# Performance work log

Measured on AMD Instinct MI355X. Metric: run time of the kernel, lower is better.

## Reference

```python
import jax, jax.numpy as jnp
import numpy as np

N_FINE = 1_000_000
N_COARSE = 250_000
K = 9            # filter extent for pos_dim=3 lattice coarsening: 2*(pos_dim+1)+1
C_IN = 64
C_OUT = 64       # nr_filters


def setup_inputs() -> dict:
    key = jax.random.key(0)
    k1, k2, k3, k4 = jax.random.split(key, 4)
    lv = jax.random.normal(k1, (N_FINE, C_IN), dtype=jnp.float32)
    # neighbor indices of each coarse vertex into the fine vertex array;
    # real lattice uses -1 for missing neighbors, emulated by masking in reference
    neighbor_idx = jax.random.randint(k2, (N_COARSE, K), 0, N_FINE, dtype=jnp.int64)
    W = jax.random.normal(k3, (K * C_IN, C_OUT), dtype=jnp.float32) * (1.0 / np.sqrt(K * C_IN))
    b = jax.random.normal(k4, (C_OUT,), dtype=jnp.float32) * 0.01
    return {"lv": lv, "neighbor_idx": neighbor_idx, "W": W, "b": b}


def reference(lv, neighbor_idx, W, b):
    # ReluCoarsen.forward: relu on lattice values, then lattice coarsening conv.
    x = jax.nn.relu(lv)                                   # [N_fine, C_in]
    valid = neighbor_idx >= 0                             # missing-neighbor mask
    idx = jnp.maximum(neighbor_idx, 0)
    gathered = x[idx]                                     # [N_coarse, K, C_in] (irregular gather)
    gathered = jnp.where(valid[:, :, None], gathered, 0.0)
    rows = gathered.reshape(gathered.shape[0], K * C_IN)  # im2row
    lv_1 = rows @ W + b                                   # [N_coarse, C_out]
    return lv_1
```

## Files before the change

### kernel.cpp

```cpp
#include <hip/hip_runtime.h>

#define N_COARSE_C 250000
#define KNB 9
#define CIN 64
#define COUT 64
#define NKK 18

typedef __attribute__((ext_vector_type(8))) short short8;
typedef __attribute__((ext_vector_type(4))) float f32x4;

__device__ __forceinline__ unsigned short f2bf(float x) {
    __bf16 h = (__bf16)x;
    return __builtin_bit_cast(unsigned short, h);
}

__global__ __launch_bounds__(512, 4) void relu_coarsen_mfma(
    const float* __restrict__ lv,
    const int*   __restrict__ nbr,
    const float* __restrict__ W,
    const float* __restrict__ bias,
    float*       __restrict__ out)
{
    __shared__ short wf[NKK * 4 * 64 * 8];

    const int tid = threadIdx.x;

    for (int p = tid; p < (576 * 64) / 2; p += 512) {
        const int n  = p & 63;
        const int k  = (p >> 6) * 2;
        const float a0 = W[k * 64 + n];
        const float a1 = W[(k + 1) * 64 + n];
        const unsigned pk = (unsigned)f2bf(a0) | ((unsigned)f2bf(a1) << 16);
        const int kk = k >> 5;
        const int gq = (k >> 3) & 3;
        const int e  = k & 7;
        const int sidx = ((kk * 4 + (n >> 4)) * 64 + gq * 16 + (n & 15)) * 8 + e;
        *reinterpret_cast<unsigned*>(&wf[sidx]) = pk;
    }
    __syncthreads();

    const int lane = tid & 63;
    const int wave = tid >> 6;
    const int m    = lane & 15;
    const int g    = lane >> 4;

    const int c0 = blockIdx.x * 128 + wave * 16;
    int c = c0 + m;
    if (c >= N_COARSE_C) c = N_COARSE_C - 1;

    int nb[KNB];
    #pragma unroll
    for (int j = 0; j < KNB; ++j) nb[j] = nbr[c * KNB + j];

    f32x4 acc[4];
    #pragma unroll
    for (int nt = 0; nt < 4; ++nt) acc[nt] = (f32x4){0.f, 0.f, 0.f, 0.f};

    #pragma unroll
    for (int kk = 0; kk < NKK; ++kk) {
        const int j  = kk >> 1;
        const int cb = ((kk & 1) << 5) + g * 8;
        const int row = nb[j];
        short8 a;
        if (row >= 0) {
            const f32x4* src = reinterpret_cast<const f32x4*>(
                lv + (size_t)row * CIN + cb);
            f32x4 v0 = src[0];
            f32x4 v1 = src[1];
            #pragma unroll
            for (int e = 0; e < 4; ++e) {
                a[e]     = (short)f2bf(fmaxf(v0[e], 0.f));
                a[e + 4] = (short)f2bf(fmaxf(v1[e], 0.f));
            }
        } else {
            #pragma unroll
            for (int e = 0; e < 8; ++e) a[e] = (short)0;
        }
        #pragma unroll
        for (int nt = 0; nt < 4; ++nt) {
            const short8 bf = *reinterpret_cast<const short8*>(
                &wf[((kk * 4 + nt) * 64 + lane) * 8]);
            acc[nt] = __builtin_amdgcn_mfma_f32_16x16x32_bf16(a, bf, acc[nt], 0, 0, 0);
        }
    }

    #pragma unroll
    for (int r = 0; r < 4; ++r) {
        const int cr = c0 + g * 4 + r;
        if (cr < N_COARSE_C) {
            #pragma unroll
            for (int nt = 0; nt < 4; ++nt) {
                const int n = nt * 16 + m;
                out[(size_t)cr * COUT + n] = acc[nt][r] + bias[n];
            }
        }
    }
}

extern "C" void kernel_launch(void* const* d_in, const int* in_sizes, int n_in,
                              void* d_out, int out_size, void* d_ws, size_t ws_size,
                              hipStream_t stream) {
    const float* lv   = (const float*)d_in[0];
    const int*   nbr  = (const int*)d_in[1];
    const float* W    = (const float*)d_in[2];
    const float* b    = (const float*)d_in[3];
    float* out = (float*)d_out;
    const int grid = (N_COARSE_C + 127) / 128;
    relu_coarsen_mfma<<<grid, 512, 0, stream>>>(lv, nbr, W, b, out);
}
```

Baseline: 417.4 us.

## Amortize weight staging over four tiles per block and software-pipeline neighbor gathers

Each block now handles four 128-row tiles, so the bf16 weight conversion into shared memory is paid once per 512 coarse rows instead of once per 128. The gather loop is manually pipelined with four in-flight neighbor rows in registers, issuing the next row's loads before the MFMAs on the current one to hide gather latency. Weight staging uses vectorized loads, and bias is hoisted into registers. The grid shrinks fourfold, which reduces parallelism, and the extra register buffers may lower occupancy.

```diff
diff --git a/kernel.cpp b/kernel.cpp
--- a/kernel.cpp
+++ b/kernel.cpp
@@ -5,6 +5,8 @@
 #define CIN 64
 #define COUT 64
 #define NKK 18
+#define G_TILES 4
+#define ROWS_PER_BLOCK 512
 
 typedef __attribute__((ext_vector_type(8))) short short8;
 typedef __attribute__((ext_vector_type(4))) float f32x4;
@@ -25,17 +27,24 @@
 
     const int tid = threadIdx.x;
 
-    for (int p = tid; p < (576 * 64) / 2; p += 512) {
-        const int n  = p & 63;
-        const int k  = (p >> 6) * 2;
-        const float a0 = W[k * 64 + n];
-        const float a1 = W[(k + 1) * 64 + n];
-        const unsigned pk = (unsigned)f2bf(a0) | ((unsigned)f2bf(a1) << 16);
+    #pragma unroll
+    for (int it = 0; it < 9; ++it) {
+        const int q  = tid + it * 512;
+        const int kp = q >> 4;
+        const int n0 = (q & 15) * 4;
+        const int k  = kp * 2;
+        f32x4 r0 = *reinterpret_cast<const f32x4*>(W + k * 64 + n0);
+        f32x4 r1 = *reinterpret_cast<const f32x4*>(W + (k + 1) * 64 + n0);
         const int kk = k >> 5;
         const int gq = (k >> 3) & 3;
         const int e  = k & 7;
-        const int sidx = ((kk * 4 + (n >> 4)) * 64 + gq * 16 + (n & 15)) * 8 + e;
-        *reinterpret_cast<unsigned*>(&wf[sidx]) = pk;
+        #pragma unroll
+        for (int i = 0; i < 4; ++i) {
+            const int n = n0 + i;
+            const unsigned pk = (unsigned)f2bf(r0[i]) | ((unsigned)f2bf(r1[i]) << 16);
+            const int sidx = ((kk * 4 + (n >> 4)) * 64 + gq * 16 + (n & 15)) * 8 + e;
+            *reinterpret_cast<unsigned*>(&wf[sidx]) = pk;
+        }
     }
     __syncthreads();
 
@@ -44,57 +53,87 @@
     const int m    = lane & 15;
     const int g    = lane >> 4;
 
-    const int c0 = blockIdx.x * 128 + wave * 16;
-    int c = c0 + m;
-    if (c >= N_COARSE_C) c = N_COARSE_C - 1;
+    float bv[4];
+    #pragma unroll
+    for (int nt = 0; nt < 4; ++nt) bv[nt] = bias[nt * 16 + m];
 
-    int nb[KNB];
-    #pragma unroll
-    for (int j = 0; j < KNB; ++j) nb[j] = nbr[c * KNB + j];
+    const int block_c0 = blockIdx.x * ROWS_PER_BLOCK;
 
-    f32x4 acc[4];
-    #pragma unroll
-    for (int nt = 0; nt < 4; ++nt) acc[nt] = (f32x4){0.f, 0.f, 0.f, 0.f};
-
-    #pragma unroll
-    for (int kk = 0; kk < NKK; ++kk) {
-        const int j  = kk >> 1;
-        const int cb = ((kk & 1) << 5) + g * 8;
-        const int row = nb[j];
-        short8 a;
-        if (row >= 0) {
-            const f32x4* src = reinterpret_cast<const f32x4*>(
-                lv + (size_t)row * CIN + cb);
-            f32x4 v0 = src[0];
-            f32x4 v1 = src[1];
-            #pragma unroll
-            for (int e = 0; e < 4; ++e) {
-                a[e]     = (short)f2bf(fmaxf(v0[e], 0.f));
-                a[e + 4] = (short)f2bf(fmaxf(v1[e], 0.f));
-            }
-        } else {
-            #pragma unroll
-            for (int e = 0; e < 8; ++e) a[e] = (short)0;
-        }
-        #pragma unroll
-        for (int nt = 0; nt < 4; ++nt) {
-            const short8 bf = *reinterpret_cast<const short8*>(
-                &wf[((kk * 4 + nt) * 64 + lane) * 8]);
-            acc[nt] = __builtin_amdgcn_mfma_f32_16x16x32_bf16(a, bf, acc[nt], 0, 0, 0);
-        }
+    #define GISSUE(S, J)                                                        \
+    {                                                                           \
+        const int rj = nb[J];                                                   \
+        const float* p = lv + (size_t)(rj < 0 ? 0 : rj) * CIN + g * 8;          \
+        va[S][0] = *reinterpret_cast<const f32x4*>(p);                          \
+        va[S][1] = *reinterpret_cast<const f32x4*>(p + 4);                      \
+        va[S][2] = *reinterpret_cast<const f32x4*>(p + 32);                     \
+        va[S][3] = *reinterpret_cast<const f32x4*>(p + 36);                     \
     }
 
-    #pragma unroll
-    for (int r = 0; r < 4; ++r) {
-        const int cr = c0 + g * 4 + r;
-        if (cr < N_COARSE_C) {
-            #pragma unroll
-            for (int nt = 0; nt < 4; ++nt) {
-                const int n = nt * 16 + m;
-                out[(size_t)cr * COUT + n] = acc[nt][r] + bias[n];
+    #define GPROC(S, J)                                                         \
+    {                                                                           \
+        short8 ae, ao;                                                          \
+        _Pragma("unroll")                                                       \
+        for (int e2 = 0; e2 < 4; ++e2) {                                        \
+            ae[e2]     = (short)f2bf(fmaxf(va[S][0][e2], 0.f));                 \
+            ae[e2 + 4] = (short)f2bf(fmaxf(va[S][1][e2], 0.f));                 \
+            ao[e2]     = (short)f2bf(fmaxf(va[S][2][e2], 0.f));                 \
+            ao[e2 + 4] = (short)f2bf(fmaxf(va[S][3][e2], 0.f));                 \
+        }                                                                       \
+        if (nb[J] < 0) { ae = (short8)0; ao = (short8)0; }                      \
+        _Pragma("unroll")                                                       \
+        for (int nt = 0; nt < 4; ++nt) {                                        \
+            const short8 be = *reinterpret_cast<const short8*>(                 \
+                &wf[(((2 * (J)) * 4 + nt) * 64 + lane) * 8]);                   \
+            acc[nt] = __builtin_amdgcn_mfma_f32_16x16x32_bf16(ae, be, acc[nt], 0, 0, 0); \
+        }                                                                       \
+        _Pragma("unroll")                                                       \
+        for (int nt = 0; nt < 4; ++nt) {                                        \
+            const short8 bo = *reinterpret_cast<const short8*>(                 \
+                &wf[(((2 * (J) + 1) * 4 + nt) * 64 + lane) * 8]);               \
+            acc[nt] = __builtin_amdgcn_mfma_f32_16x16x32_bf16(ao, bo, acc[nt], 0, 0, 0); \
+        }                                                                       \
+    }
+
+    #pragma unroll 1
+    for (int t = 0; t < G_TILES; ++t) {
+        const int c0 = block_c0 + t * 128 + wave * 16;
+        int c = c0 + m;
+        if (c >= N_COARSE_C) c = N_COARSE_C - 1;
+
+        int nb[KNB];
+        #pragma unroll
+        for (int j = 0; j < KNB; ++j) nb[j] = nbr[c * KNB + j];
+
+        f32x4 acc[4];
+        #pragma unroll
+        for (int nt = 0; nt < 4; ++nt) acc[nt] = (f32x4){0.f, 0.f, 0.f, 0.f};
+
+        f32x4 va[4][4];
+
+        GISSUE(0, 0) GISSUE(1, 1) GISSUE(2, 2) GISSUE(3, 3)
+        GPROC(0, 0) GISSUE(0, 4)
+        GPROC(1, 1) GISSUE(1, 5)
+        GPROC(2, 2) GISSUE(2, 6)
+        GPROC(3, 3) GISSUE(3, 7)
+        GPROC(0, 4) GISSUE(0, 8)
+        GPROC(1, 5)
+        GPROC(2, 6)
+        GPROC(3, 7)
+        GPROC(0, 8)
+
+        #pragma unroll
+        for (int r = 0; r < 4; ++r) {
+            const int cr = c0 + g * 4 + r;
+            if (cr < N_COARSE_C) {
+                #pragma unroll
+                for (int nt = 0; nt < 4; ++nt) {
+                    out[(size_t)cr * COUT + nt * 16 + m] = acc[nt][r] + bv[nt];
+                }
             }
         }
     }
+    #undef GISSUE
+    #undef GPROC
 }
 
 extern "C" void kernel_launch(void* const* d_in, const int* in_sizes, int n_in,
@@ -105,6 +144,6 @@
     const float* W    = (const float*)d_in[2];
     const float* b    = (const float*)d_in[3];
     float* out = (float*)d_out;
-    const int grid = (N_COARSE_C + 127) / 128;
+    const int grid = (N_COARSE_C + ROWS_PER_BLOCK - 1) / ROWS_PER_BLOCK;
     relu_coarsen_mfma<<<grid, 512, 0, stream>>>(lv, nbr, W, b, out);
 }
```

Result: slower. 607.1 us (+45.4%).
